# Performance work log

Hardware: AMD Instinct MI355X
Metric: run time of the kernel (lower is better)

Reference implementation:

```python
import jax, jax.numpy as jnp
import numpy as np

IN_DIM = 3
GRID_LEVEL = 7
FEAT_DIMS = 2
HIDDEN = 128
BOUND = 1.0
W0_SINE = 56.0  # n_levels**feature_dims - n_levels = 8**2 - 8
N = 131072


def setup_inputs() -> dict:
    key = jax.random.key(0)
    ks = jax.random.split(key, 10)
    return {
        "in_pos": jax.random.uniform(ks[0], (N, IN_DIM), jnp.float32, -1.0, 1.0),
        "grid_feats": jax.random.uniform(ks[1], (N, IN_DIM + GRID_LEVEL * FEAT_DIMS), jnp.float32),
        "ffn_A": jax.random.normal(ks[2], (GRID_LEVEL, FEAT_DIMS, HIDDEN), jnp.float32) * 5.0,
        "ffn_sigma": jnp.ones((GRID_LEVEL,), jnp.float32),
        "W0": jax.random.uniform(ks[3], (HIDDEN, IN_DIM), jnp.float32, -1.0 / IN_DIM, 1.0 / IN_DIM),
        "b0": jax.random.uniform(ks[4], (HIDDEN,), jnp.float32, -1.0 / IN_DIM, 1.0 / IN_DIM),
        "W_mid": jax.random.uniform(ks[5], (GRID_LEVEL, HIDDEN, HIDDEN), jnp.float32) * (2.0 * np.sqrt(6.0 / HIDDEN) / W0_SINE) - np.sqrt(6.0 / HIDDEN) / W0_SINE,
        "b_mid": jnp.zeros((GRID_LEVEL, HIDDEN), jnp.float32),
        "W_high": jax.random.uniform(ks[6], (GRID_LEVEL, HIDDEN, HIDDEN), jnp.float32) * (2.0 * np.sqrt(6.0 / HIDDEN) / W0_SINE) - np.sqrt(6.0 / HIDDEN) / W0_SINE,
        "b_high": jnp.zeros((GRID_LEVEL, HIDDEN), jnp.float32),
    }


def reference(in_pos, grid_feats, ffn_A, ffn_sigma, W0, b0, W_mid, b_mid, W_high, b_high):
    x = in_pos / BOUND                     # [N, 3], in [-1, 1]
    pos01 = (in_pos + BOUND) / (2.0 * BOUND)  # [N, 3], in [0, 1]

    # grid branch: slice off the first in_dim columns, reshape to [L, N, F]
    gx = grid_feats[..., IN_DIM:].reshape(-1, GRID_LEVEL, FEAT_DIMS).transpose(1, 0, 2)
    A = ffn_A * ffn_sigma[:, None, None]   # [L, F, H]
    grid_x = jnp.sin(jnp.einsum('lnf,lfh->lnh', gx, (2.0 * jnp.pi) * A))  # [L, N, H]

    # first SIREN layer
    x = jnp.sin(W0_SINE * (x @ W0.T + b0))  # [N, H]

    def step(carry, layer):
        x, buf = carry
        Wm, bm, Wh, bh, g = layer
        x = jnp.sin(W0_SINE * (x @ Wm.T + bm))
        x = g + x                                  # residual add of grid features
        buf = buf + jnp.sin(W0_SINE * (x @ Wh.T + bh))  # high-freq accumulation
        return (x, buf), None

    buf0 = jnp.zeros((x.shape[0], HIDDEN), x.dtype)
    (_, buf), _ = jax.lax.scan(step, (x, buf0), (W_mid, b_mid, W_high, b_high, grid_x))

    return jnp.concatenate([pos01, buf / GRID_LEVEL], axis=-1)  # [N, 3 + 128]
```

## Files before the change

kernel.cpp:

```cpp
#include <hip/hip_runtime.h>
#include <hip/hip_bf16.h>


typedef __bf16 bf16_t;
typedef __attribute__((ext_vector_type(8))) __bf16 bf16x8;
typedef __attribute__((ext_vector_type(4))) float f32x4;
typedef __attribute__((ext_vector_type(16))) float f32x16;

#define C56R 8.9126768f
#define INV7 0.14285714285714285f

#define OFF_WMF   0
#define OFF_WMFLO 229376
#define OFF_WHF   458752
#define OFF_EPM   688128

union ChunkU { bf16x8 v; unsigned int d[4]; };

__device__ __forceinline__ unsigned short bfbits(float x) {
  bf16_t b = (bf16_t)x;
  return __builtin_bit_cast(unsigned short, b);
}
__device__ __forceinline__ float bf2f(unsigned short u) {
  return __builtin_bit_cast(float, (unsigned int)u << 16);
}
__device__ __forceinline__ void pack2(float v0, float v1,
                                      unsigned int& ph, unsigned int& pl) {
  unsigned short h0 = bfbits(v0), h1 = bfbits(v1);
  ph = (unsigned int)h0 | ((unsigned int)h1 << 16);
  float l0 = v0 - bf2f(h0), l1 = v1 - bf2f(h1);
  pl = (unsigned int)bfbits(l0) | ((unsigned int)bfbits(l1) << 16);
}
__device__ __forceinline__ void stage16(const void* g, void* l) {
  __builtin_amdgcn_global_load_lds(
      (const __attribute__((address_space(1))) unsigned int*)g,
      (__attribute__((address_space(3))) unsigned int*)l, 16, 0, 0);
}

__global__ void ffb_prep(const float* __restrict__ ffnA, const float* __restrict__ sigma,
                         const float* __restrict__ Wm, const float* __restrict__ bm,
                         const float* __restrict__ Wh, const float* __restrict__ bh,
                         unsigned char* __restrict__ ws) {
  int i = blockIdx.x * 256 + threadIdx.x;
  bf16_t* wmf = (bf16_t*)(ws + OFF_WMF);
  bf16_t* wml = (bf16_t*)(ws + OFF_WMFLO);
  bf16_t* whf = (bf16_t*)(ws + OFF_WHF);
  {
    int j    = i & 7;
    int lane = (i >> 3) & 63;
    int kc   = (i >> 9) & 7;
    int mt   = (i >> 12) & 3;
    int it   = i >> 14;
    int ho   = (mt << 5) + (lane & 31);
    int hin  = (kc << 4) + ((lane >> 5) << 3) + j;
    int src  = (it << 14) + (ho << 7) + hin;
    float w  = Wm[src];
    bf16_t h = (bf16_t)w;
    wmf[i] = h;
    wml[i] = (bf16_t)(w - (float)h);
    whf[i] = (bf16_t)Wh[src];
  }
  if (i < 896) {
    int r  = i & 15;
    int mt = (i >> 4) & 3;
    int hf = (i >> 6) & 1;
    int it = i >> 7;
    int h  = (mt << 5) + (r & 3) + ((r >> 2) << 3) + (hf << 2);
    float sg = sigma[it];
    f32x4 e;
    e.x = ffnA[it * 256 + h] * sg;
    e.y = ffnA[it * 256 + 128 + h] * sg;
    e.z = C56R * bm[it * 128 + h];
    e.w = C56R * bh[it * 128 + h];
    ((f32x4*)(ws + OFF_EPM))[i] = e;
  }
}

__launch_bounds__(512, 4)
__global__ void ffb_main(const float* __restrict__ pos,
                         const float* __restrict__ gfeat,
                         const float* __restrict__ W0,
                         const float* __restrict__ b0,
                         const unsigned char* __restrict__ ws,
                         float* __restrict__ out) {
  __shared__ __align__(16) unsigned char smem[65536];

  const int tid  = threadIdx.x;
  const int L    = tid & 63;
  const int wave = tid >> 6;
  const int qd   = wave >> 2;
  const int sub  = wave & 3;
  const int p    = L & 31;
  const int hf   = L >> 5;
  const int n    = (blockIdx.x << 6) + (qd << 5) + p;

  unsigned char* sMH = smem;
  unsigned char* sX  = smem + 32768 + (qd << 14);

  const bf16_t* __restrict__ WML = (const bf16_t*)(ws + OFF_WMFLO);
  const bf16_t* __restrict__ WHF = (const bf16_t*)(ws + OFF_WHF);
  const f32x4*  __restrict__ EPM = (const f32x4*)(ws + OFF_EPM);
  const float*  __restrict__ EPW = (const float*)(ws + OFF_EPM);

  {
    const unsigned char* src = ws + OFF_WMF + (wave << 12) + (L << 4);
    unsigned char* dst = sMH + (wave << 12);
    #pragma unroll
    for (int c = 0; c < 4; ++c)
      stage16(src + (c << 10), dst + (c << 10));
  }

  const float p0 = pos[n * 3 + 0], p1 = pos[n * 3 + 1], p2 = pos[n * 3 + 2];
  if (sub == 0 && hf == 0) {
    out[n * 131 + 0] = (p0 + 1.f) * 0.5f;
    out[n * 131 + 1] = (p1 + 1.f) * 0.5f;
    out[n * 131 + 2] = (p2 + 1.f) * 0.5f;
  }

  #pragma unroll
  for (int cc = 0; cc < 2; ++cc) {
    const int c = (sub << 1) + cc;
    ChunkU chi, clo;
    #pragma unroll
    for (int jp = 0; jp < 4; ++jp) {
      int h0 = (c << 4) + (hf << 3) + 2 * jp;
      float d0 = __builtin_fmaf(p2, W0[h0*3+2], __builtin_fmaf(p1, W0[h0*3+1], p0 * W0[h0*3+0]));
      float d1 = __builtin_fmaf(p2, W0[h0*3+5], __builtin_fmaf(p1, W0[h0*3+4], p0 * W0[h0*3+3]));
      float v0 = __builtin_amdgcn_sinf(C56R * (d0 + b0[h0]));
      float v1 = __builtin_amdgcn_sinf(C56R * (d1 + b0[h0 + 1]));
      pack2(v0, v1, chi.d[jp], clo.d[jp]);
    }
    *(bf16x8*)(sX + (c << 10) + (L << 4))        = chi.v;
    *(bf16x8*)(sX + 8192 + (c << 10) + (L << 4)) = clo.v;
  }
  __syncthreads();

  f32x16 buf;
  #pragma unroll
  for (int r = 0; r < 16; ++r) buf[r] = 0.f;

  for (int it = 0; it < 8; ++it) {
    if (it > 0) {
      f32x16 acc;
      #pragma unroll
      for (int r = 0; r < 16; ++r) acc[r] = 0.f;
      const bf16_t* wb = WHF + ((it - 1) << 14) + (sub << 12) + (L << 3);
      bf16x8 fnext = *(const bf16x8*)(wb);
      #pragma unroll
      for (int kc = 0; kc < 8; ++kc) {
        bf16x8 f = fnext;
        if (kc < 7) fnext = *(const bf16x8*)(wb + ((kc + 1) << 9));
        bf16x8 xhc = *(const bf16x8*)(sX + (kc << 10) + (L << 4));
        acc = __builtin_amdgcn_mfma_f32_32x32x16_bf16(f, xhc, acc, 0, 0, 0);
      }
      const int eb = ((((it - 1) << 1) + hf) << 2) + sub;
      #pragma unroll
      for (int r = 0; r < 16; ++r) {
        float cbh = EPW[(eb * 16 + r) * 4 + 3];
        buf[r] += __builtin_amdgcn_sinf(__builtin_fmaf(acc[r], C56R, cbh));
      }
    }

    if (it < 7) {
      f32x16 acc;
      #pragma unroll
      for (int r = 0; r < 16; ++r) acc[r] = 0.f;
      const bf16_t* wl = WML + (it << 14) + (sub << 12) + (L << 3);
      const unsigned char* smh = sMH + (sub << 13) + (L << 4);
      bf16x8 flnext = *(const bf16x8*)(wl);
      #pragma unroll
      for (int kc = 0; kc < 8; ++kc) {
        bf16x8 fl = flnext;
        if (kc < 7) flnext = *(const bf16x8*)(wl + ((kc + 1) << 9));
        bf16x8 fh  = *(const bf16x8*)(smh + (kc << 10));
        bf16x8 xhc = *(const bf16x8*)(sX + (kc << 10) + (L << 4));
        bf16x8 xlc = *(const bf16x8*)(sX + 8192 + (kc << 10) + (L << 4));
        acc = __builtin_amdgcn_mfma_f32_32x32x16_bf16(fh, xhc, acc, 0, 0, 0);
        acc = __builtin_amdgcn_mfma_f32_32x32x16_bf16(fl, xhc, acc, 0, 0, 0);
        acc = __builtin_amdgcn_mfma_f32_32x32x16_bf16(fh, xlc, acc, 0, 0, 0);
      }

      __syncthreads();

      if (it < 6) {
        const unsigned char* src = ws + OFF_WMF + ((it + 1) << 15) + (wave << 12) + (L << 4);
        unsigned char* dst = sMH + (wave << 12);
        #pragma unroll
        for (int c = 0; c < 4; ++c)
          stage16(src + (c << 10), dst + (c << 10));
      }

      const float g0 = gfeat[n * 17 + 3 + 2 * it];
      const float g1 = gfeat[n * 17 + 4 + 2 * it];
      const int eb = (((it << 1) + hf) << 2) + sub;
      #pragma unroll
      for (int rp = 0; rp < 8; ++rp) {
        const int r = 2 * rp;
        f32x4 e0 = EPM[eb * 16 + r];
        f32x4 e1 = EPM[eb * 16 + r + 1];
        float sg0 = __builtin_amdgcn_sinf(__builtin_amdgcn_fractf(__builtin_fmaf(g1, e0.y, g0 * e0.x)));
        float sg1 = __builtin_amdgcn_sinf(__builtin_amdgcn_fractf(__builtin_fmaf(g1, e1.y, g0 * e1.x)));
        float sm0 = __builtin_amdgcn_sinf(__builtin_fmaf(acc[r],     C56R, e0.z));
        float sm1 = __builtin_amdgcn_sinf(__builtin_fmaf(acc[r + 1], C56R, e1.z));
        unsigned int phv, plv;
        pack2(sg0 + sm0, sg1 + sm1, phv, plv);
        const int h   = (sub << 5) + (r & 3) + ((r >> 2) << 3) + (hf << 2);
        const int off = ((h >> 4) << 10) + ((p + (((h >> 3) & 1) << 5)) << 4) + ((h & 7) << 1);
        *(unsigned int*)(sX + off)        = phv;
        *(unsigned int*)(sX + 8192 + off) = plv;
      }
      __syncthreads();
    }
  }

  float* op = out + (size_t)n * 131 + 3;
  #pragma unroll
  for (int r = 0; r < 16; ++r) {
    const int h = (sub << 5) + (r & 3) + ((r >> 2) << 3) + (hf << 2);
    op[h] = buf[r] * INV7;
  }
}

extern "C" void kernel_launch(void* const* d_in, const int* in_sizes, int n_in,
                              void* d_out, int out_size, void* d_ws, size_t ws_size,
                              hipStream_t stream) {
  (void)in_sizes; (void)n_in; (void)out_size; (void)ws_size;
  const float* pos   = (const float*)d_in[0];
  const float* gfeat = (const float*)d_in[1];
  const float* ffnA  = (const float*)d_in[2];
  const float* sigma = (const float*)d_in[3];
  const float* W0    = (const float*)d_in[4];
  const float* b0    = (const float*)d_in[5];
  const float* Wm    = (const float*)d_in[6];
  const float* bm    = (const float*)d_in[7];
  const float* Wh    = (const float*)d_in[8];
  const float* bh    = (const float*)d_in[9];
  float* out = (float*)d_out;
  unsigned char* ws = (unsigned char*)d_ws;

  hipLaunchKernelGGL(ffb_prep, dim3(448), dim3(256), 0, stream,
                     ffnA, sigma, Wm, bm, Wh, bh, ws);
  hipLaunchKernelGGL(ffb_main, dim3(2048), dim3(512), 0, stream,
                     pos, gfeat, W0, b0, ws, out);
}
```

Baseline: 285.1 us.

## Fuse high and mid MFMA loops per step and shrink blocks to 32 points

```diff
diff --git a/kernel.cpp b/kernel.cpp
--- a/kernel.cpp
+++ b/kernel.cpp
@@ -76,26 +76,23 @@
   }
 }
 
-__launch_bounds__(512, 4)
+__launch_bounds__(256, 3)
 __global__ void ffb_main(const float* __restrict__ pos,
                          const float* __restrict__ gfeat,
                          const float* __restrict__ W0,
                          const float* __restrict__ b0,
                          const unsigned char* __restrict__ ws,
                          float* __restrict__ out) {
-  __shared__ __align__(16) unsigned char smem[65536];
-
-  const int tid  = threadIdx.x;
-  const int L    = tid & 63;
-  const int wave = tid >> 6;
-  const int qd   = wave >> 2;
-  const int sub  = wave & 3;
-  const int p    = L & 31;
-  const int hf   = L >> 5;
-  const int n    = (blockIdx.x << 6) + (qd << 5) + p;
-
+  __shared__ __align__(16) unsigned char smem[49152];
   unsigned char* sMH = smem;
-  unsigned char* sX  = smem + 32768 + (qd << 14);
+  unsigned char* sX  = smem + 32768;
+
+  const int tid = threadIdx.x;
+  const int L   = tid & 63;
+  const int sub = tid >> 6;
+  const int p   = L & 31;
+  const int hf  = L >> 5;
+  const int n   = (blockIdx.x << 5) + p;
 
   const bf16_t* __restrict__ WML = (const bf16_t*)(ws + OFF_WMFLO);
   const bf16_t* __restrict__ WHF = (const bf16_t*)(ws + OFF_WHF);
@@ -103,11 +100,10 @@
   const float*  __restrict__ EPW = (const float*)(ws + OFF_EPM);
 
   {
-    const unsigned char* src = ws + OFF_WMF + (wave << 12) + (L << 4);
-    unsigned char* dst = sMH + (wave << 12);
-    #pragma unroll
-    for (int c = 0; c < 4; ++c)
-      stage16(src + (c << 10), dst + (c << 10));
+    const unsigned char* src = ws + OFF_WMF + (sub << 13) + (L << 4);
+    unsigned char* dst = sMH + (sub << 13);
+    #pragma unroll
+    for (int c = 0; c < 8; ++c) stage16(src + (c << 10), dst + (c << 10));
   }
 
   const float p0 = pos[n * 3 + 0], p1 = pos[n * 3 + 1], p2 = pos[n * 3 + 2];
@@ -140,58 +136,62 @@
   for (int r = 0; r < 16; ++r) buf[r] = 0.f;
 
   for (int it = 0; it < 8; ++it) {
-    if (it > 0) {
-      f32x16 acc;
+    const bool doHigh = (it > 0);
+    const bool doMid  = (it < 7);
+
+    float g0 = 0.f, g1 = 0.f;
+    if (doMid) {
+      g0 = gfeat[n * 17 + 3 + 2 * it];
+      g1 = gfeat[n * 17 + 4 + 2 * it];
+    }
+
+    f32x16 accm, acch;
+    #pragma unroll
+    for (int r = 0; r < 16; ++r) { accm[r] = 0.f; acch[r] = 0.f; }
+    const bf16_t* wl = WML + (it << 14) + (sub << 12) + (L << 3);
+    const bf16_t* wb = WHF + ((it - 1) << 14) + (sub << 12) + (L << 3);
+    const unsigned char* smh = sMH + (sub << 13) + (L << 4);
+    bf16x8 fl_n, wb_n;
+    if (doMid)  fl_n = *(const bf16x8*)(wl);
+    if (doHigh) wb_n = *(const bf16x8*)(wb);
+    #pragma unroll
+    for (int kc = 0; kc < 8; ++kc) {
+      bf16x8 flv = fl_n, wbv = wb_n;
+      if (kc < 7) {
+        if (doMid)  fl_n = *(const bf16x8*)(wl + ((kc + 1) << 9));
+        if (doHigh) wb_n = *(const bf16x8*)(wb + ((kc + 1) << 9));
+      }
+      bf16x8 xh = *(const bf16x8*)(sX + (kc << 10) + (L << 4));
+      if (doHigh)
+        acch = __builtin_amdgcn_mfma_f32_32x32x16_bf16(wbv, xh, acch, 0, 0, 0);
+      if (doMid) {
+        bf16x8 fh = *(const bf16x8*)(smh + (kc << 10));
+        bf16x8 xl = *(const bf16x8*)(sX + 8192 + (kc << 10) + (L << 4));
+        accm = __builtin_amdgcn_mfma_f32_32x32x16_bf16(fh, xh, accm, 0, 0, 0);
+        accm = __builtin_amdgcn_mfma_f32_32x32x16_bf16(flv, xh, accm, 0, 0, 0);
+        accm = __builtin_amdgcn_mfma_f32_32x32x16_bf16(fh, xl, accm, 0, 0, 0);
+      }
+    }
+
+    if (it < 6) {
+      __builtin_amdgcn_s_waitcnt(0xC07F);
+      const unsigned char* src = ws + OFF_WMF + ((it + 1) << 15) + (sub << 13) + (L << 4);
+      unsigned char* dst = sMH + (sub << 13);
       #pragma unroll
-      for (int r = 0; r < 16; ++r) acc[r] = 0.f;
-      const bf16_t* wb = WHF + ((it - 1) << 14) + (sub << 12) + (L << 3);
-      bf16x8 fnext = *(const bf16x8*)(wb);
-      #pragma unroll
-      for (int kc = 0; kc < 8; ++kc) {
-        bf16x8 f = fnext;
-        if (kc < 7) fnext = *(const bf16x8*)(wb + ((kc + 1) << 9));
-        bf16x8 xhc = *(const bf16x8*)(sX + (kc << 10) + (L << 4));
-        acc = __builtin_amdgcn_mfma_f32_32x32x16_bf16(f, xhc, acc, 0, 0, 0);
-      }
+      for (int c = 0; c < 8; ++c) stage16(src + (c << 10), dst + (c << 10));
+    }
+
+    if (doHigh) {
       const int eb = ((((it - 1) << 1) + hf) << 2) + sub;
       #pragma unroll
       for (int r = 0; r < 16; ++r) {
         float cbh = EPW[(eb * 16 + r) * 4 + 3];
-        buf[r] += __builtin_amdgcn_sinf(__builtin_fmaf(acc[r], C56R, cbh));
-      }
-    }
-
-    if (it < 7) {
-      f32x16 acc;
-      #pragma unroll
-      for (int r = 0; r < 16; ++r) acc[r] = 0.f;
-      const bf16_t* wl = WML + (it << 14) + (sub << 12) + (L << 3);
-      const unsigned char* smh = sMH + (sub << 13) + (L << 4);
-      bf16x8 flnext = *(const bf16x8*)(wl);
-      #pragma unroll
-      for (int kc = 0; kc < 8; ++kc) {
-        bf16x8 fl = flnext;
-        if (kc < 7) flnext = *(const bf16x8*)(wl + ((kc + 1) << 9));
-        bf16x8 fh  = *(const bf16x8*)(smh + (kc << 10));
-        bf16x8 xhc = *(const bf16x8*)(sX + (kc << 10) + (L << 4));
-        bf16x8 xlc = *(const bf16x8*)(sX + 8192 + (kc << 10) + (L << 4));
-        acc = __builtin_amdgcn_mfma_f32_32x32x16_bf16(fh, xhc, acc, 0, 0, 0);
-        acc = __builtin_amdgcn_mfma_f32_32x32x16_bf16(fl, xhc, acc, 0, 0, 0);
-        acc = __builtin_amdgcn_mfma_f32_32x32x16_bf16(fh, xlc, acc, 0, 0, 0);
-      }
-
+        buf[r] += __builtin_amdgcn_sinf(__builtin_fmaf(acch[r], C56R, cbh));
+      }
+    }
+
+    if (doMid) {
       __syncthreads();
-
-      if (it < 6) {
-        const unsigned char* src = ws + OFF_WMF + ((it + 1) << 15) + (wave << 12) + (L << 4);
-        unsigned char* dst = sMH + (wave << 12);
-        #pragma unroll
-        for (int c = 0; c < 4; ++c)
-          stage16(src + (c << 10), dst + (c << 10));
-      }
-
-      const float g0 = gfeat[n * 17 + 3 + 2 * it];
-      const float g1 = gfeat[n * 17 + 4 + 2 * it];
       const int eb = (((it << 1) + hf) << 2) + sub;
       #pragma unroll
       for (int rp = 0; rp < 8; ++rp) {
@@ -200,8 +200,8 @@
         f32x4 e1 = EPM[eb * 16 + r + 1];
         float sg0 = __builtin_amdgcn_sinf(__builtin_amdgcn_fractf(__builtin_fmaf(g1, e0.y, g0 * e0.x)));
         float sg1 = __builtin_amdgcn_sinf(__builtin_amdgcn_fractf(__builtin_fmaf(g1, e1.y, g0 * e1.x)));
-        float sm0 = __builtin_amdgcn_sinf(__builtin_fmaf(acc[r],     C56R, e0.z));
-        float sm1 = __builtin_amdgcn_sinf(__builtin_fmaf(acc[r + 1], C56R, e1.z));
+        float sm0 = __builtin_amdgcn_sinf(__builtin_fmaf(accm[r],     C56R, e0.z));
+        float sm1 = __builtin_amdgcn_sinf(__builtin_fmaf(accm[r + 1], C56R, e1.z));
         unsigned int phv, plv;
         pack2(sg0 + sm0, sg1 + sm1, phv, plv);
         const int h   = (sub << 5) + (r & 3) + ((r >> 2) << 3) + (hf << 2);
@@ -240,6 +240,6 @@
 
   hipLaunchKernelGGL(ffb_prep, dim3(448), dim3(256), 0, stream,
                      ffnA, sigma, Wm, bm, Wh, bh, ws);
-  hipLaunchKernelGGL(ffb_main, dim3(2048), dim3(512), 0, stream,
+  hipLaunchKernelGGL(ffb_main, dim3(4096), dim3(256), 0, stream,
                      pos, gfeat, W0, b0, ws, out);
 }
```

After: 389.6 us. 1.37x slower.
